# Performance work log

Measured on AMD Instinct MI355X. Metric: run time of the kernel, lower is better.

Reference implementation:

```python
import jax, jax.numpy as jnp
import numpy as np

N = 100000      # total nodes = B_GRAPHS * NODES_PER_GRAPH
NPG = 1000      # nodes per graph (num_nodes in module)
B_GRAPHS = 100
H = 128         # hidden_channels
CIN = 3         # in_channels
E = 1600000     # edges (avg_degree 16)
OUT = 2         # out_channels


def setup_inputs() -> dict:
    key = jax.random.key(0)
    ks = jax.random.split(key, 20)
    s = 0.05
    inp = {
        "x": jax.random.normal(ks[0], (N, CIN), jnp.float32),
        "edge_index": jnp.stack([
            jax.random.randint(ks[1], (E,), 0, N),
            jax.random.randint(ks[2], (E,), 0, N),
        ]).astype(jnp.int64),
        "batch": jnp.repeat(jnp.arange(B_GRAPHS), NPG).astype(jnp.int64),
        # DiffusionConv layer 0: CIN -> H ; layer 1: H -> H
        "W_self0": jax.random.normal(ks[3], (CIN, H), jnp.float32) * s,
        "W_nbr0": jax.random.normal(ks[4], (CIN, H), jnp.float32) * s,
        "b0": jnp.zeros((H,), jnp.float32),
        "W_self1": jax.random.normal(ks[5], (H, H), jnp.float32) * s,
        "W_nbr1": jax.random.normal(ks[6], (H, H), jnp.float32) * s,
        "b1": jnp.zeros((H,), jnp.float32),
        # 2 stacked LSTMs (torch layout: W_ih [4H, in], W_hh [4H, H])
        "Wih0": jax.random.normal(ks[7], (4 * H, H), jnp.float32) * s,
        "Whh0": jax.random.normal(ks[8], (4 * H, H), jnp.float32) * s,
        "bih0": jnp.zeros((4 * H,), jnp.float32),
        "bhh0": jnp.zeros((4 * H,), jnp.float32),
        "Wih1": jax.random.normal(ks[9], (4 * H, H), jnp.float32) * s,
        "Whh1": jax.random.normal(ks[10], (4 * H, H), jnp.float32) * s,
        "bih1": jnp.zeros((4 * H,), jnp.float32),
        "bhh1": jnp.zeros((4 * H,), jnp.float32),
        # output head
        "W_out": jax.random.normal(ks[11], (H, OUT), jnp.float32) * s,
        "b_out": jnp.zeros((OUT,), jnp.float32),
    }
    return inp


def diffusion_conv(h, src, dst, W_self, W_nbr, b):
    # gather-aggregate-transform: out = h W_self + (D^-1 A h) W_nbr + b
    msgs = h[src]                                            # [E, C] gather
    agg = jax.ops.segment_sum(msgs, dst, num_segments=N)     # [N, C] scatter-add
    deg = jax.ops.segment_sum(jnp.ones((src.shape[0], 1), h.dtype), dst,
                              num_segments=N)                # [N, 1]
    agg = agg / jnp.maximum(deg, 1.0)
    return h @ W_self + agg @ W_nbr + b


def lstm_layer(x_seq, Wih, Whh, bih, bhh):
    # x_seq: [T, Bn, H] seq-first, zero initial state (torch default)
    Bn = x_seq.shape[1]
    h0 = jnp.zeros((Bn, H), x_seq.dtype)
    c0 = jnp.zeros((Bn, H), x_seq.dtype)

    def step(carry, xt):
        h, c = carry
        g = xt @ Wih.T + h @ Whh.T + (bih + bhh)   # [Bn, 4H]
        i, f, gg, o = jnp.split(g, 4, axis=-1)     # torch gate order i,f,g,o
        c = jax.nn.sigmoid(f) * c + jax.nn.sigmoid(i) * jnp.tanh(gg)
        h = jax.nn.sigmoid(o) * jnp.tanh(c)
        return (h, c), h

    _, hs = jax.lax.scan(step, (h0, c0), x_seq)
    return hs


def reference(x, edge_index, batch, W_self0, W_nbr0, b0, W_self1, W_nbr1, b1,
              Wih0, Whh0, bih0, bhh0, Wih1, Whh1, bih1, bhh1, W_out, b_out):
    src, dst = edge_index[0], edge_index[1]
    h = jax.nn.relu(diffusion_conv(x, src, dst, W_self0, W_nbr0, b0))
    h = jax.nn.relu(diffusion_conv(h, src, dst, W_self1, W_nbr1, b1))
    # view(-1, num_nodes, hidden): [B_GRAPHS, NPG, H], LSTM seq-first
    seq = h.reshape(B_GRAPHS, NPG, H)
    seq = lstm_layer(seq, Wih0, Whh0, bih0, bhh0)
    seq = lstm_layer(seq, Wih1, Whh1, bih1, bhh1)
    h = seq.reshape(N, H)
    # global_mean_pool over batch vector
    pooled = jax.ops.segment_sum(h, batch, num_segments=B_GRAPHS)
    cnt = jax.ops.segment_sum(jnp.ones((N, 1), h.dtype), batch,
                              num_segments=B_GRAPHS)
    pooled = pooled / jnp.maximum(cnt, 1.0)
    logits = pooled @ W_out + b_out                # [B_GRAPHS, OUT]
    return jax.nn.log_softmax(logits, axis=1)
```

## Files before the change

kernel.cpp:

```cpp
#include <hip/hip_runtime.h>

#define N_NODES 100000
#define NPG     1000
#define B_GR    100
#define HDIM    128
#define E_EDGES 1600000

typedef __attribute__((ext_vector_type(8))) short bf16x8;
typedef __attribute__((ext_vector_type(4))) float f32x4;
typedef unsigned long long u64;
typedef unsigned short u16;

__device__ __forceinline__ float sigf(float x) { return 1.f / (1.f + __expf(-x)); }
__device__ __forceinline__ float tanh_fast(float x) { return 1.f - 2.f / (__expf(2.f * x) + 1.f); }
__device__ __forceinline__ u16 f2bf(float f) {
    unsigned u = __float_as_uint(f);
    unsigned r = (u + 0x7fffu + ((u >> 16) & 1u)) >> 16;
    return (u16)r;
}
__device__ __forceinline__ float bf2f(u16 h) { return __uint_as_float(((unsigned)h) << 16); }
__device__ __forceinline__ f32x4 MF(bf16x8 a, bf16x8 b, f32x4 c) {
    return __builtin_amdgcn_mfma_f32_16x16x32_bf16(a, b, c, 0, 0, 0);
}
__device__ __forceinline__ u64 pack4(f32x4 a) {
    return (u64)f2bf(a[0]) | ((u64)f2bf(a[1]) << 16)
         | ((u64)f2bf(a[2]) << 32) | ((u64)f2bf(a[3]) << 48);
}

__global__ void k_build(const int* __restrict__ src, const int* __restrict__ dst,
                        int* __restrict__ cnt, int* __restrict__ ell) {
    int e = blockIdx.x * 256 + threadIdx.x;
    if (e >= E_EDGES) return;
    int d = dst[e];
    int pos = atomicAdd(&cnt[d], 1);
    if (pos < 64) ell[(size_t)d * 64 + pos] = src[e];
}

__global__ __launch_bounds__(256)
void k_conv0w(const float* __restrict__ x, const int* __restrict__ cnt, const int* __restrict__ ell,
              const float* __restrict__ Ws, const float* __restrict__ Wn, const float* __restrict__ b,
              u16* __restrict__ Hbf) {
    int n = blockIdx.x * 4 + (threadIdx.x >> 6);
    int lane = threadIdx.x & 63;
    if (n >= N_NODES) return;
    int degt = cnt[n];
    int deg = min(degt, 64);
    float a0 = 0.f, a1 = 0.f, a2 = 0.f;
    if (lane < deg) {
        int s = ell[(size_t)n * 64 + lane];
        a0 = x[s * 3 + 0]; a1 = x[s * 3 + 1]; a2 = x[s * 3 + 2];
    }
#pragma unroll
    for (int off = 1; off < 64; off <<= 1) {
        a0 += __shfl_xor(a0, off);
        a1 += __shfl_xor(a1, off);
        a2 += __shfl_xor(a2, off);
    }
    float inv = 1.f / fmaxf((float)degt, 1.f);
    a0 *= inv; a1 *= inv; a2 *= inv;
    float x0 = x[n * 3 + 0], x1 = x[n * 3 + 1], x2 = x[n * 3 + 2];
#pragma unroll
    for (int q = 0; q < 2; ++q) {
        int c = lane + 64 * q;
        float acc = b[c]
            + x0 * Ws[c] + x1 * Ws[128 + c] + x2 * Ws[256 + c]
            + a0 * Wn[c] + a1 * Wn[128 + c] + a2 * Wn[256 + c];
        Hbf[(size_t)n * 128 + c] = f2bf(fmaxf(acc, 0.f));
    }
}

__global__ __launch_bounds__(256)
void k_agg2e(const u16* __restrict__ hin, const int* __restrict__ cnt, const int* __restrict__ ell,
             u16* __restrict__ out) {
    int wid = threadIdx.x >> 6;
    int l = threadIdx.x & 63;
    int n = blockIdx.x * 4 + wid;
    if (n >= N_NODES) return;
    int degt = cnt[n];
    int deg = min(degt, 64);
    int myidx = ell[(size_t)n * 64 + l];
    float ax = 0.f, ay = 0.f;
    const unsigned* base = (const unsigned*)hin;
    int j = 0;
    for (; j + 4 <= deg; j += 4) {
        int i0 = __shfl(myidx, j);
        int i1 = __shfl(myidx, j + 1);
        int i2 = __shfl(myidx, j + 2);
        int i3 = __shfl(myidx, j + 3);
        unsigned v0 = base[(size_t)i0 * 64 + l];
        unsigned v1 = base[(size_t)i1 * 64 + l];
        unsigned v2 = base[(size_t)i2 * 64 + l];
        unsigned v3 = base[(size_t)i3 * 64 + l];
        ax += bf2f((u16)v0); ay += bf2f((u16)(v0 >> 16));
        ax += bf2f((u16)v1); ay += bf2f((u16)(v1 >> 16));
        ax += bf2f((u16)v2); ay += bf2f((u16)(v2 >> 16));
        ax += bf2f((u16)v3); ay += bf2f((u16)(v3 >> 16));
    }
    for (; j < deg; ++j) {
        int i0 = __shfl(myidx, j);
        unsigned v = base[(size_t)i0 * 64 + l];
        ax += bf2f((u16)v); ay += bf2f((u16)(v >> 16));
    }
    float dv = fmaxf((float)degt, 1.f);
    unsigned o = (unsigned)f2bf(ax / dv) | ((unsigned)f2bf(ay / dv) << 16);
    *(unsigned*)&out[(size_t)n * 128 + l * 2] = o;
}

__global__ __launch_bounds__(256)
void k_conv1mm(const u16* __restrict__ Hbf, const u16* __restrict__ AGbf,
               const float* __restrict__ Wself, const float* __restrict__ Wnbr,
               const float* __restrict__ bias, u16* __restrict__ Xf) {
    __shared__ float As[64 * 64];
    __shared__ float Wls[64 * 128];
    int tid = threadIdx.x;
    int r0 = blockIdx.x * 64;
    int tx = tid & 31, ty = tid >> 5;
    float acc[8][4];
#pragma unroll
    for (int r = 0; r < 8; ++r)
#pragma unroll
        for (int j = 0; j < 4; ++j) acc[r][j] = 0.f;

    for (int chunk = 0; chunk < 4; ++chunk) {
        const u16* Abf = (chunk < 2) ? Hbf : AGbf;
        const float* Wsrc = (chunk < 2) ? Wself : Wnbr;
        int k0 = (chunk & 1) * 64;
#pragma unroll
        for (int i = 0; i < 4; ++i) {
            int e = tid + 256 * i;
            int row = e >> 4, c4 = e & 15;
            int grow = r0 + row;
            float4 v = make_float4(0.f, 0.f, 0.f, 0.f);
            if (grow < N_NODES) {
                u64 p = *(const u64*)&Abf[(size_t)grow * 128 + k0 + c4 * 4];
                v.x = bf2f((u16)p);         v.y = bf2f((u16)(p >> 16));
                v.z = bf2f((u16)(p >> 32)); v.w = bf2f((u16)(p >> 48));
            }
            *(float4*)&As[row * 64 + c4 * 4] = v;
        }
#pragma unroll
        for (int i = 0; i < 8; ++i) {
            int e = tid + 256 * i;
            int row = e >> 5, c4 = e & 31;
            *(float4*)&Wls[row * 128 + c4 * 4] = *(const float4*)&Wsrc[(k0 + row) * 128 + c4 * 4];
        }
        __syncthreads();
#pragma unroll 4
        for (int kk = 0; kk < 64; ++kk) {
            float4 w = *(const float4*)&Wls[kk * 128 + tx * 4];
#pragma unroll
            for (int r = 0; r < 8; ++r) {
                float a = As[(ty + 8 * r) * 64 + kk];
                acc[r][0] += a * w.x; acc[r][1] += a * w.y;
                acc[r][2] += a * w.z; acc[r][3] += a * w.w;
            }
        }
        __syncthreads();
    }
    float4 bb = *(const float4*)&bias[tx * 4];
    int col0 = tx * 4;
#pragma unroll
    for (int r = 0; r < 8; ++r) {
        int grow = r0 + ty + 8 * r;
        if (grow < N_NODES) {
            u16 h0 = f2bf(fmaxf(acc[r][0] + bb.x, 0.f));
            u16 h1 = f2bf(fmaxf(acc[r][1] + bb.y, 0.f));
            u16 h2 = f2bf(fmaxf(acc[r][2] + bb.z, 0.f));
            u16 h3 = f2bf(fmaxf(acc[r][3] + bb.w, 0.f));
            u64 pk = (u64)h0 | ((u64)h1 << 16) | ((u64)h2 << 32) | ((u64)h3 << 48);
            int t = grow / 1000;
            int rv = grow - t * 1000;
            int rb2 = rv >> 4, rr = rv & 15;
            size_t idx = (size_t)(t * 63 + rb2) * 2048
                       + (size_t)((col0 >> 5) * 512 + ((col0 >> 3) & 3) * 128 + rr * 8 + (col0 & 7));
            *(u64*)(Xf + idx) = pk;
        }
    }
}

__global__ void k_prepf(const float* __restrict__ Wih0, const float* __restrict__ Whh0,
                        const float* __restrict__ Wih1, const float* __restrict__ Whh1,
                        u16* __restrict__ WTf) {
    int idx = blockIdx.x * 256 + threadIdx.x;
    int lane = idx & 63;
    int gt = (idx >> 6) & 3;
    int kt = (idx >> 8) & 7;
    int w  = (idx >> 11) & 7;
    int l  = idx >> 14;
    int d = 16 * w + (lane & 15);
    int k0 = kt * 32 + (lane >> 4) * 8;
    int wrow = gt * 128 + d;
    const float* Wi = l ? Wih1 : Wih0;
    const float* Wh = l ? Whh1 : Whh0;
    const float* srcp = (k0 < 128) ? (Wi + wrow * 128 + k0) : (Wh + wrow * 128 + (k0 - 128));
    u16 o[8];
#pragma unroll
    for (int j = 0; j < 8; ++j) o[j] = f2bf(srcp[j]);
    u64* dst = (u64*)(WTf + (size_t)idx * 8);
    dst[0] = (u64)o[0] | ((u64)o[1] << 16) | ((u64)o[2] << 32) | ((u64)o[3] << 48);
    dst[1] = (u64)o[4] | ((u64)o[5] << 16) | ((u64)o[6] << 32) | ((u64)o[7] << 48);
}

__global__ void k_bsum(const float* __restrict__ bih0, const float* __restrict__ bhh0,
                       const float* __restrict__ bih1, const float* __restrict__ bhh1,
                       float* __restrict__ bs) {
    int i = blockIdx.x * 256 + threadIdx.x;
    int l = i >> 9, c = i & 511;
    bs[i] = l ? (bih1[c] + bhh1[c]) : (bih0[c] + bhh0[c]);
}

__global__ __launch_bounds__(512, 1)
void k_gemmA(const u16* __restrict__ src, const u16* __restrict__ WTf,
             const float* __restrict__ bsB, u16* __restrict__ Gx, int t0, int layer) {
    extern __shared__ __align__(16) u16 smem[];
    int tid = threadIdx.x;
    int l = tid & 63, w = tid >> 6;
    int rb = blockIdx.x % 63;
    int slice = blockIdx.x / 63;
    {
        const u64* Wsrc = (const u64*)(WTf + (size_t)layer * 131072);
        u64* Wd = (u64*)smem;
#pragma unroll
        for (int i = 0; i < 32; ++i) {
            int j = tid + i * 512;
            int dfrag = j >> 7, r = j & 127;
            int w_ = dfrag >> 4, kt2 = (dfrag >> 2) & 3, gt = dfrag & 3;
            int gfrag = (w_ * 8 + kt2) * 4 + gt;
            Wd[j] = Wsrc[(size_t)gfrag * 128 + r];
        }
    }
    __syncthreads();
    int d = (w << 4) | (l & 15);
    float b0v = bsB[layer * 512 + d];
    float b1v = bsB[layer * 512 + 128 + d];
    float b2v = bsB[layer * 512 + 256 + d];
    float b3v = bsB[layer * 512 + 384 + d];
    const u16* wbase = smem + (size_t)w * 8192 + l * 8;
    for (int tt = 0; tt < 10; ++tt) {
        int t = t0 + slice * 10 + tt;
        const u16* xb = src + ((size_t)t * 63 + rb) * 2048 + l * 8;
        bf16x8 x0 = *(const bf16x8*)(xb);
        bf16x8 x1 = *(const bf16x8*)(xb + 512);
        bf16x8 x2 = *(const bf16x8*)(xb + 1024);
        bf16x8 x3 = *(const bf16x8*)(xb + 1536);
        f32x4 a0 = {b0v, b0v, b0v, b0v};
        f32x4 a1 = {b1v, b1v, b1v, b1v};
        f32x4 a2 = {b2v, b2v, b2v, b2v};
        f32x4 a3 = {b3v, b3v, b3v, b3v};
#pragma unroll
        for (int kt2 = 0; kt2 < 4; ++kt2) {
            bf16x8 xa = (kt2 == 0) ? x0 : (kt2 == 1) ? x1 : (kt2 == 2) ? x2 : x3;
            a0 = MF(xa, *(const bf16x8*)(wbase + (kt2 * 4 + 0) * 512), a0);
            a1 = MF(xa, *(const bf16x8*)(wbase + (kt2 * 4 + 1) * 512), a1);
            a2 = MF(xa, *(const bf16x8*)(wbase + (kt2 * 4 + 2) * 512), a2);
            a3 = MF(xa, *(const bf16x8*)(wbase + (kt2 * 4 + 3) * 512), a3);
        }
        size_t gbase = ((size_t)(t - t0) * 63 + rb) * 8192 + (size_t)w * 1024 + l * 4;
        *(u64*)(Gx + gbase)       = pack4(a0);
        *(u64*)(Gx + gbase + 256) = pack4(a1);
        *(u64*)(Gx + gbase + 512) = pack4(a2);
        *(u64*)(Gx + gbase + 768) = pack4(a3);
    }
}

__global__ __launch_bounds__(512, 1)
void k_recB(const u16* __restrict__ Gx, const u16* __restrict__ WTf,
            u16* __restrict__ H0f, float* __restrict__ pooled,
            u16* __restrict__ hstate, float* __restrict__ cstate,
            int t0, int layer) {
    extern __shared__ __align__(16) u16 smem[];
    u16* Wlds = smem;
    u16* hshA = smem + 65536;
    u16* hshB = smem + 67584;
    int tid = threadIdx.x;
    int l = tid & 63, w = tid >> 6;
    int rb = blockIdx.x;

    {
        u64 hv = (t0 == 0) ? 0ull : ((const u64*)(hstate + (size_t)rb * 2048))[tid];
        ((u64*)hshA)[tid] = hv;
    }
    {
        const u64* Wsrc = (const u64*)(WTf + (size_t)layer * 131072);
        u64* Wd = (u64*)Wlds;
#pragma unroll
        for (int i = 0; i < 32; ++i) {
            int j = tid + i * 512;
            int dfrag = j >> 7, r = j & 127;
            int w_ = dfrag >> 4, kt2 = (dfrag >> 2) & 3, gt = dfrag & 3;
            int gfrag = (w_ * 8 + 4 + kt2) * 4 + gt;
            Wd[j] = Wsrc[(size_t)gfrag * 128 + r];
        }
    }
    float cst0, cst1, cst2, cst3;
    if (t0 == 0) {
        cst0 = cst1 = cst2 = cst3 = 0.f;
    } else {
        const f32x4 cv = *(const f32x4*)(cstate + ((size_t)rb * 512 + tid) * 4);
        cst0 = cv[0]; cst1 = cv[1]; cst2 = cv[2]; cst3 = cv[3];
    }
    __syncthreads();

    int d = (w << 4) | (l & 15);
    int ktp = d >> 5, oct = (d >> 3) & 3, boff = d & 7;
    int hbase = ktp * 512 + ((l >> 4) * 4 + 16 * oct) * 8 + boff;
    const u16* wbase = Wlds + (size_t)w * 8192 + l * 8;
    int n0 = rb * 16;
    int nreal = min(16, NPG - n0);
    int cur = 0;

    for (int tt = 0; tt < 50; ++tt) {
        int t = t0 + tt;
        size_t gbase = ((size_t)tt * 63 + rb) * 8192 + (size_t)w * 1024 + l * 4;
        u64 p0 = *(const u64*)(Gx + gbase);
        u64 p1 = *(const u64*)(Gx + gbase + 256);
        u64 p2 = *(const u64*)(Gx + gbase + 512);
        u64 p3 = *(const u64*)(Gx + gbase + 768);

        const u16* hc = cur ? hshB : hshA;
        u16* hn = cur ? hshA : hshB;
        f32x4 a0 = {0.f, 0.f, 0.f, 0.f};
        f32x4 a1 = {0.f, 0.f, 0.f, 0.f};
        f32x4 a2 = {0.f, 0.f, 0.f, 0.f};
        f32x4 a3 = {0.f, 0.f, 0.f, 0.f};
#pragma unroll
        for (int kt2 = 0; kt2 < 4; ++kt2) {
            bf16x8 hf = *(const bf16x8*)(hc + kt2 * 512 + l * 8);
            a0 = MF(hf, *(const bf16x8*)(wbase + (kt2 * 4 + 0) * 512), a0);
            a1 = MF(hf, *(const bf16x8*)(wbase + (kt2 * 4 + 1) * 512), a1);
            a2 = MF(hf, *(const bf16x8*)(wbase + (kt2 * 4 + 2) * 512), a2);
            a3 = MF(hf, *(const bf16x8*)(wbase + (kt2 * 4 + 3) * 512), a3);
        }
        float hsum = 0.f;
#pragma unroll
        for (int reg = 0; reg < 4; ++reg) {
            float gi = a0[reg] + bf2f((u16)(p0 >> (16 * reg)));
            float gf = a1[reg] + bf2f((u16)(p1 >> (16 * reg)));
            float gg = a2[reg] + bf2f((u16)(p2 >> (16 * reg)));
            float go = a3[reg] + bf2f((u16)(p3 >> (16 * reg)));
            float cprev = (reg == 0) ? cst0 : (reg == 1) ? cst1 : (reg == 2) ? cst2 : cst3;
            float c = sigf(gf) * cprev + sigf(gi) * tanh_fast(gg);
            if (reg == 0) cst0 = c; else if (reg == 1) cst1 = c;
            else if (reg == 2) cst2 = c; else cst3 = c;
            float h = sigf(go) * tanh_fast(c);
            u16 hb = f2bf(h);
            hn[hbase + reg * 8] = hb;
            if (layer == 0) {
                H0f[((size_t)t * 63 + rb) * 2048 + hbase + reg * 8] = hb;
            } else {
                int row = (l >> 4) * 4 + reg;
                if (row < nreal) hsum += h;
            }
        }
        if (layer == 1) {
            hsum += __shfl_xor(hsum, 16);
            hsum += __shfl_xor(hsum, 32);
            if ((l >> 4) == 0) atomicAdd(&pooled[t * 128 + d], hsum);
        }
        __syncthreads();
        cur ^= 1;
    }
    ((u64*)(hstate + (size_t)rb * 2048))[tid] = ((const u64*)(cur ? hshB : hshA))[tid];
    f32x4 cv = {cst0, cst1, cst2, cst3};
    *(f32x4*)(cstate + ((size_t)rb * 512 + tid) * 4) = cv;
}

__global__ void k_head(const float* __restrict__ pooled, const float* __restrict__ Wout,
                       const float* __restrict__ bout, float* __restrict__ out) {
    int gi = threadIdx.x;
    if (gi >= B_GR) return;
    float l0 = bout[0], l1 = bout[1];
    for (int d = 0; d < 128; ++d) {
        float p = pooled[gi * 128 + d] / 1000.0f;
        l0 += p * Wout[d * 2 + 0];
        l1 += p * Wout[d * 2 + 1];
    }
    float m = fmaxf(l0, l1);
    float lse = m + logf(__expf(l0 - m) + __expf(l1 - m));
    out[gi * 2 + 0] = l0 - lse;
    out[gi * 2 + 1] = l1 - lse;
}

extern "C" void kernel_launch(void* const* d_in, const int* in_sizes, int n_in,
                              void* d_out, int out_size, void* d_ws, size_t ws_size,
                              hipStream_t stream) {
    const float* x    = (const float*)d_in[0];
    const int*   ei   = (const int*)d_in[1];
    const int*   srcI = ei;
    const int*   dstI = ei + E_EDGES;
    const float* Ws0  = (const float*)d_in[3];
    const float* Wn0  = (const float*)d_in[4];
    const float* b0   = (const float*)d_in[5];
    const float* Ws1  = (const float*)d_in[6];
    const float* Wn1  = (const float*)d_in[7];
    const float* b1   = (const float*)d_in[8];
    const float* Wih0 = (const float*)d_in[9];
    const float* Whh0 = (const float*)d_in[10];
    const float* bih0 = (const float*)d_in[11];
    const float* bhh0 = (const float*)d_in[12];
    const float* Wih1 = (const float*)d_in[13];
    const float* Whh1 = (const float*)d_in[14];
    const float* bih1 = (const float*)d_in[15];
    const float* bhh1 = (const float*)d_in[16];
    const float* Wout = (const float*)d_in[17];
    const float* bout = (const float*)d_in[18];
    float* out = (float*)d_out;

    char* ws = (char*)d_ws;
    int*   cnt    = (int*)(ws + 0);
    int*   ell    = (int*)(ws + 400128);
    u16*   Hbf    = (u16*)(ws + 26000128);
    u16*   AGbf   = (u16*)(ws + 51600128);
    u16*   Xf     = (u16*)(ws + 77414400);
    u16*   WTf    = (u16*)(ws + 103219200);
    float* bsB    = (float*)(ws + 103743488);
    float* pooled = (float*)(ws + 103747584);
    u16*   hstate = (u16*)(ws + 103798784);
    float* cstate = (float*)(ws + 104056832);
    u16*   H0f    = (u16*)(ws + 0);
    u16*   Gx     = (u16*)(ws + 25804800);

    hipMemsetAsync(cnt, 0, 400128, stream);
    hipMemsetAsync(pooled, 0, B_GR * 128 * sizeof(float), stream);

    k_build<<<E_EDGES / 256, 256, 0, stream>>>(srcI, dstI, cnt, ell);
    k_conv0w<<<N_NODES / 4, 256, 0, stream>>>(x, cnt, ell, Ws0, Wn0, b0, Hbf);
    k_agg2e<<<N_NODES / 4, 256, 0, stream>>>(Hbf, cnt, ell, AGbf);
    k_conv1mm<<<(N_NODES + 63) / 64, 256, 0, stream>>>(Hbf, AGbf, Ws1, Wn1, b1, Xf);

    k_prepf<<<128, 256, 0, stream>>>(Wih0, Whh0, Wih1, Whh1, WTf);
    k_bsum<<<4, 256, 0, stream>>>(bih0, bhh0, bih1, bhh1, bsB);

    hipFuncSetAttribute((const void*)k_gemmA, hipFuncAttributeMaxDynamicSharedMemorySize, 131072);
    hipFuncSetAttribute((const void*)k_recB,  hipFuncAttributeMaxDynamicSharedMemorySize, 139264);

    for (int layer = 0; layer < 2; ++layer) {
        const u16* srcT = layer ? H0f : Xf;
        for (int half = 0; half < 2; ++half) {
            int t0 = half * 50;
            k_gemmA<<<315, 512, 131072, stream>>>(srcT, WTf, bsB, Gx, t0, layer);
            k_recB<<<63, 512, 139264, stream>>>(Gx, WTf, H0f, pooled, hstate, cstate, t0, layer);
        }
    }

    k_head<<<1, 128, 0, stream>>>(pooled, Wout, bout, out);
}
```

Baseline: 869.7 us.

## Move conv1 transform to bf16 MFMA with split weights and partition edge build by destination

Replaces the FP32 scalar tiled GEMM for the second diffusion conv with an MFMA kernel. A prep kernel splits the concatenated self/neighbour weights into bf16 hi and lo parts and lays them out as MFMA fragments kept in 128KB of LDS. Each wave multiplies 16-row groups against both weight parts to keep near-fp32 accuracy. Separately, the ELL build now makes 8 passes over the edges, each handling only one destination range, to improve atomic and write locality at the cost of reading dst eight times.

```diff
diff --git a/kernel.cpp b/kernel.cpp
--- a/kernel.cpp
+++ b/kernel.cpp
@@ -27,13 +27,21 @@
          | ((u64)f2bf(a[2]) << 32) | ((u64)f2bf(a[3]) << 48);
 }
 
-__global__ void k_build(const int* __restrict__ src, const int* __restrict__ dst,
-                        int* __restrict__ cnt, int* __restrict__ ell) {
-    int e = blockIdx.x * 256 + threadIdx.x;
-    if (e >= E_EDGES) return;
-    int d = dst[e];
-    int pos = atomicAdd(&cnt[d], 1);
-    if (pos < 64) ell[(size_t)d * 64 + pos] = src[e];
+__global__ void k_build8(const int* __restrict__ src, const int* __restrict__ dst,
+                         int* __restrict__ cnt, int* __restrict__ ell) {
+    int tid0 = blockIdx.x * 256 + threadIdx.x;
+#pragma unroll 1
+    for (int p = 0; p < 8; ++p) {
+        int lo = p * 12500, hi = lo + 12500;
+#pragma unroll 1
+        for (int e = tid0; e < E_EDGES; e += 256 * 256) {
+            int d = dst[e];
+            if (d >= lo && d < hi) {
+                int pos = atomicAdd(&cnt[d], 1);
+                if (pos < 64) ell[(size_t)d * 64 + pos] = src[e];
+            }
+        }
+    }
 }
 
 __global__ __launch_bounds__(256)
@@ -106,74 +114,89 @@
     *(unsigned*)&out[(size_t)n * 128 + l * 2] = o;
 }
 
-__global__ __launch_bounds__(256)
-void k_conv1mm(const u16* __restrict__ Hbf, const u16* __restrict__ AGbf,
-               const float* __restrict__ Wself, const float* __restrict__ Wnbr,
-               const float* __restrict__ bias, u16* __restrict__ Xf) {
-    __shared__ float As[64 * 64];
-    __shared__ float Wls[64 * 128];
+__global__ void k_prepc(const float* __restrict__ Wself, const float* __restrict__ Wnbr,
+                        u16* __restrict__ WCf) {
+    int idx = blockIdx.x * 256 + threadIdx.x;
+    int fi = idx & 4095;
+    int lo = idx >> 12;
+    int lane = fi & 63;
+    int colt = (fi >> 6) & 7;
+    int kt = fi >> 9;
+    int col = colt * 16 + (lane & 15);
+    int k0 = kt * 32 + (lane >> 4) * 8;
+    u16 o[8];
+#pragma unroll
+    for (int j = 0; j < 8; ++j) {
+        int k = k0 + j;
+        float v = (k < 128) ? Wself[k * 128 + col] : Wnbr[(k - 128) * 128 + col];
+        u16 hi = f2bf(v);
+        o[j] = lo ? f2bf(v - bf2f(hi)) : hi;
+    }
+    u64* dst = (u64*)(WCf + (size_t)idx * 8);
+    dst[0] = (u64)o[0] | ((u64)o[1] << 16) | ((u64)o[2] << 32) | ((u64)o[3] << 48);
+    dst[1] = (u64)o[4] | ((u64)o[5] << 16) | ((u64)o[6] << 32) | ((u64)o[7] << 48);
+}
+
+__global__ __launch_bounds__(256, 1)
+void k_conv1f(const u16* __restrict__ Hbf, const u16* __restrict__ AGbf,
+              const u16* __restrict__ WCf, const float* __restrict__ bias,
+              u16* __restrict__ Xf) {
+    extern __shared__ __align__(16) u16 smem[];
     int tid = threadIdx.x;
-    int r0 = blockIdx.x * 64;
-    int tx = tid & 31, ty = tid >> 5;
-    float acc[8][4];
-#pragma unroll
-    for (int r = 0; r < 8; ++r)
-#pragma unroll
-        for (int j = 0; j < 4; ++j) acc[r][j] = 0.f;
-
-    for (int chunk = 0; chunk < 4; ++chunk) {
-        const u16* Abf = (chunk < 2) ? Hbf : AGbf;
-        const float* Wsrc = (chunk < 2) ? Wself : Wnbr;
-        int k0 = (chunk & 1) * 64;
-#pragma unroll
-        for (int i = 0; i < 4; ++i) {
-            int e = tid + 256 * i;
-            int row = e >> 4, c4 = e & 15;
-            int grow = r0 + row;
-            float4 v = make_float4(0.f, 0.f, 0.f, 0.f);
-            if (grow < N_NODES) {
-                u64 p = *(const u64*)&Abf[(size_t)grow * 128 + k0 + c4 * 4];
-                v.x = bf2f((u16)p);         v.y = bf2f((u16)(p >> 16));
-                v.z = bf2f((u16)(p >> 32)); v.w = bf2f((u16)(p >> 48));
+    int l = tid & 63, w = tid >> 6;
+    {
+        const u64* Wsrc = (const u64*)WCf;
+        u64* Wd = (u64*)smem;
+#pragma unroll
+        for (int i = 0; i < 64; ++i)
+            Wd[tid + 256 * i] = Wsrc[tid + 256 * i];
+    }
+    __syncthreads();
+    int r0 = blockIdx.x * 256 + w * 64;
+
+#pragma unroll 1
+    for (int g = 0; g < 4; ++g) {
+        int rowA = r0 + g * 16 + (l & 15);
+        int row = min(rowA, N_NODES - 1);
+        int koff = (l >> 4) * 8;
+        bf16x8 act[8];
+#pragma unroll
+        for (int kt = 0; kt < 4; ++kt) {
+            act[kt]     = *(const bf16x8*)(Hbf  + (size_t)row * 128 + kt * 32 + koff);
+            act[4 + kt] = *(const bf16x8*)(AGbf + (size_t)row * 128 + kt * 32 + koff);
+        }
+        f32x4 acc[8];
+#pragma unroll
+        for (int c = 0; c < 8; ++c) acc[c] = (f32x4){0.f, 0.f, 0.f, 0.f};
+#pragma unroll
+        for (int kt = 0; kt < 8; ++kt)
+#pragma unroll
+            for (int colt = 0; colt < 8; ++colt) {
+                bf16x8 wf = *(const bf16x8*)(smem + ((kt * 8 + colt) * 64 + l) * 8);
+                acc[colt] = MF(wf, act[kt], acc[colt]);
             }
-            *(float4*)&As[row * 64 + c4 * 4] = v;
-        }
-#pragma unroll
-        for (int i = 0; i < 8; ++i) {
-            int e = tid + 256 * i;
-            int row = e >> 5, c4 = e & 31;
-            *(float4*)&Wls[row * 128 + c4 * 4] = *(const float4*)&Wsrc[(k0 + row) * 128 + c4 * 4];
-        }
-        __syncthreads();
-#pragma unroll 4
-        for (int kk = 0; kk < 64; ++kk) {
-            float4 w = *(const float4*)&Wls[kk * 128 + tx * 4];
-#pragma unroll
-            for (int r = 0; r < 8; ++r) {
-                float a = As[(ty + 8 * r) * 64 + kk];
-                acc[r][0] += a * w.x; acc[r][1] += a * w.y;
-                acc[r][2] += a * w.z; acc[r][3] += a * w.w;
+#pragma unroll
+        for (int kt = 0; kt < 8; ++kt)
+#pragma unroll
+            for (int colt = 0; colt < 8; ++colt) {
+                bf16x8 wf = *(const bf16x8*)(smem + 32768 + ((kt * 8 + colt) * 64 + l) * 8);
+                acc[colt] = MF(wf, act[kt], acc[colt]);
             }
-        }
-        __syncthreads();
-    }
-    float4 bb = *(const float4*)&bias[tx * 4];
-    int col0 = tx * 4;
-#pragma unroll
-    for (int r = 0; r < 8; ++r) {
-        int grow = r0 + ty + 8 * r;
-        if (grow < N_NODES) {
-            u16 h0 = f2bf(fmaxf(acc[r][0] + bb.x, 0.f));
-            u16 h1 = f2bf(fmaxf(acc[r][1] + bb.y, 0.f));
-            u16 h2 = f2bf(fmaxf(acc[r][2] + bb.z, 0.f));
-            u16 h3 = f2bf(fmaxf(acc[r][3] + bb.w, 0.f));
-            u64 pk = (u64)h0 | ((u64)h1 << 16) | ((u64)h2 << 32) | ((u64)h3 << 48);
-            int t = grow / 1000;
-            int rv = grow - t * 1000;
+        if (rowA < N_NODES) {
+            int t = rowA / 1000;
+            int rv = rowA - t * 1000;
             int rb2 = rv >> 4, rr = rv & 15;
-            size_t idx = (size_t)(t * 63 + rb2) * 2048
-                       + (size_t)((col0 >> 5) * 512 + ((col0 >> 3) & 3) * 128 + rr * 8 + (col0 & 7));
-            *(u64*)(Xf + idx) = pk;
+            size_t tilebase = (size_t)(t * 63 + rb2) * 2048 + rr * 8;
+#pragma unroll
+            for (int colt = 0; colt < 8; ++colt) {
+                int col0 = colt * 16 + ((l >> 4) << 2);
+                f32x4 v;
+#pragma unroll
+                for (int reg = 0; reg < 4; ++reg)
+                    v[reg] = fmaxf(acc[colt][reg] + bias[col0 + reg], 0.f);
+                size_t idx = tilebase + (size_t)((col0 >> 5) * 512 + ((col0 >> 3) & 3) * 128 + (col0 & 7));
+                *(u64*)(Xf + idx) = pack4(v);
+            }
         }
     }
 }
@@ -417,22 +440,26 @@
     float* pooled = (float*)(ws + 103747584);
     u16*   hstate = (u16*)(ws + 103798784);
     float* cstate = (float*)(ws + 104056832);
+    u16*   WCf    = (u16*)(ws + 104572928);
     u16*   H0f    = (u16*)(ws + 0);
     u16*   Gx     = (u16*)(ws + 25804800);
 
     hipMemsetAsync(cnt, 0, 400128, stream);
     hipMemsetAsync(pooled, 0, B_GR * 128 * sizeof(float), stream);
 
-    k_build<<<E_EDGES / 256, 256, 0, stream>>>(srcI, dstI, cnt, ell);
+    k_build8<<<256, 256, 0, stream>>>(srcI, dstI, cnt, ell);
     k_conv0w<<<N_NODES / 4, 256, 0, stream>>>(x, cnt, ell, Ws0, Wn0, b0, Hbf);
     k_agg2e<<<N_NODES / 4, 256, 0, stream>>>(Hbf, cnt, ell, AGbf);
-    k_conv1mm<<<(N_NODES + 63) / 64, 256, 0, stream>>>(Hbf, AGbf, Ws1, Wn1, b1, Xf);
+    k_prepc<<<32, 256, 0, stream>>>(Ws1, Wn1, WCf);
+
+    hipFuncSetAttribute((const void*)k_conv1f, hipFuncAttributeMaxDynamicSharedMemorySize, 131072);
+    hipFuncSetAttribute((const void*)k_gemmA,  hipFuncAttributeMaxDynamicSharedMemorySize, 131072);
+    hipFuncSetAttribute((const void*)k_recB,   hipFuncAttributeMaxDynamicSharedMemorySize, 139264);
+
+    k_conv1f<<<(N_NODES + 255) / 256, 256, 131072, stream>>>(Hbf, AGbf, WCf, b1, Xf);
 
     k_prepf<<<128, 256, 0, stream>>>(Wih0, Whh0, Wih1, Whh1, WTf);
     k_bsum<<<4, 256, 0, stream>>>(bih0, bhh0, bih1, bhh1, bsB);
-
-    hipFuncSetAttribute((const void*)k_gemmA, hipFuncAttributeMaxDynamicSharedMemorySize, 131072);
-    hipFuncSetAttribute((const void*)k_recB,  hipFuncAttributeMaxDynamicSharedMemorySize, 139264);
 
     for (int layer = 0; layer < 2; ++layer) {
         const u16* srcT = layer ? H0f : Xf;
```

Result: slower. 911.1 us (+4.8%).
